# Kernel optimization log

Hardware: AMD Instinct MI355X
Metric: run time of the kernel (lower is better)

## Reference

```python
import jax, jax.numpy as jnp
import numpy as np

SLOPE = 25.0  # snntorch fast_sigmoid default slope
ALPHA = 1.0   # gradient-reversal strength (forward default)

@jax.custom_vjp
def fs_spike(x):
    return (x > 0).astype(x.dtype)
def _fs_fwd(x):
    return (x > 0).astype(x.dtype), x
def _fs_bwd(x, g):
    return (g / (SLOPE * jnp.abs(x) + 1.0) ** 2,)
fs_spike.defvjp(_fs_fwd, _fs_bwd)

@jax.custom_vjp
def atan_spike(x):  # snntorch default ATan surrogate (alpha=2)
    return (x > 0).astype(x.dtype)
def _at_fwd(x):
    return (x > 0).astype(x.dtype), x
def _at_bwd(x, g):
    return (g / (1.0 + (jnp.pi * x) ** 2),)
atan_spike.defvjp(_at_fwd, _at_bwd)

@jax.custom_vjp
def grad_reverse(x):
    return x
def _gr_fwd(x):
    return x, None
def _gr_bwd(_, g):
    return (-ALPHA * g,)
grad_reverse.defvjp(_gr_fwd, _gr_bwd)

def lstm_cell(x, h, c, w_ih, w_hh, b_ih, b_hh):
    gates = x @ w_ih.T + b_ih + h @ w_hh.T + b_hh
    i, f, g, o = jnp.split(gates, 4, axis=-1)
    c_new = jax.nn.sigmoid(f) * c + jax.nn.sigmoid(i) * jnp.tanh(g)
    h_new = jax.nn.sigmoid(o) * jnp.tanh(c_new)
    return h_new, c_new

def slstm_step(x, syn, mem, w_ih, w_hh, b_ih, b_hh, thr):
    # reset computed from previous mem, detached (snntorch mem_reset)
    reset = jax.lax.stop_gradient((mem - thr > 0).astype(mem.dtype))
    h, c = lstm_cell(x, mem, syn, w_ih, w_hh, b_ih, b_hh)
    mem_new = h - reset * thr  # reset_mechanism='subtract'
    spk = fs_spike(mem_new - thr)
    return spk, c, mem_new

def _forward(x, conv_w, bn_gamma, bn_beta, thr_lif1,
             w_ih1, w_hh1, b_ih1, b_hh1, thr1,
             w_ih2, w_hh2, b_ih2, b_hh2, thr2,
             fc_g_w, fc_g_b, fc_d1_w, fc_d1_b, thr_dom, fc_d2_w, fc_d2_b):
    T, B, C = x.shape
    xc = jnp.transpose(x, (1, 2, 0))  # [B, C, T]
    conv = jax.lax.conv_general_dilated(xc, conv_w, window_strides=(1,),
                                        padding=[(2, 2)],
                                        dimension_numbers=('NCH', 'OIH', 'NCH'))
    # BatchNorm1d in training mode: batch stats over (B, T) per channel
    mu = conv.mean(axis=(0, 2), keepdims=True)
    var = conv.var(axis=(0, 2), keepdims=True)
    bn = (conv - mu) / jnp.sqrt(var + 1e-5) * bn_gamma[None, :, None] + bn_beta[None, :, None]
    # Leaky neuron, single step from zero mem: mem = input, spk = fire(mem - thr)
    spk_conv = atan_spike(bn - thr_lif1)
    seq = jnp.transpose(spk_conv, (2, 0, 1))  # [T, B, 64]
    H = w_hh1.shape[1]
    init = (jnp.zeros((B, H), x.dtype), jnp.zeros((B, H), x.dtype),
            jnp.zeros((B, H), x.dtype), jnp.zeros((B, H), x.dtype))

    def step(carry, xt):
        syn1, mem1, syn2, mem2 = carry
        spk1, syn1, mem1 = slstm_step(xt, syn1, mem1, w_ih1, w_hh1, b_ih1, b_hh1, thr1)
        spk2, syn2, mem2 = slstm_step(spk1, syn2, mem2, w_ih2, w_hh2, b_ih2, b_hh2, thr2)
        return (syn1, mem1, syn2, mem2), mem2

    _, mem2_rec = jax.lax.scan(step, init, seq)  # [T, B, H]
    features = mem2_rec.mean(axis=0)             # [B, H]
    gesture = features @ fc_g_w.T + fc_g_b
    rev = grad_reverse(features)
    domain_hidden = atan_spike(rev @ fc_d1_w.T + fc_d1_b - thr_dom)
    domain = domain_hidden @ fc_d2_w.T + fc_d2_b
    return gesture, domain

def setup_inputs() -> dict:
    key = jax.random.key(0)
    ks = jax.random.split(key, 16)
    T, B, C, H = 2000, 256, 14, 128
    f = jnp.float32
    return {
        'x': jax.random.normal(ks[0], (T, B, C), f),
        'conv_w': jax.random.normal(ks[1], (64, C, 5), f) * 0.12,
        'bn_gamma': jnp.ones((64,), f),
        'bn_beta': jnp.zeros((64,), f),
        'thr_lif1': jnp.ones((), f),
        'w_ih1': jax.random.normal(ks[2], (4 * H, 64), f) * 0.08,
        'w_hh1': jax.random.normal(ks[3], (4 * H, H), f) * 0.08,
        'b_ih1': jnp.zeros((4 * H,), f),
        'b_hh1': jnp.zeros((4 * H,), f),
        'thr1': jnp.ones((), f),
        'w_ih2': jax.random.normal(ks[4], (4 * H, H), f) * 0.08,
        'w_hh2': jax.random.normal(ks[5], (4 * H, H), f) * 0.08,
        'b_ih2': jnp.zeros((4 * H,), f),
        'b_hh2': jnp.zeros((4 * H,), f),
        'thr2': jnp.ones((), f),
        'fc_g_w': jax.random.normal(ks[6], (8, H), f) * 0.08,
        'fc_g_b': jnp.zeros((8,), f),
        'fc_d1_w': jax.random.normal(ks[7], (64, H), f) * 0.08,
        'fc_d1_b': jnp.zeros((64,), f),
        'thr_dom': jnp.ones((), f),
        'fc_d2_w': jax.random.normal(ks[8], (10, 64), f) * 0.1,
        'fc_d2_b': jnp.zeros((10,), f),
    }

def reference(x, conv_w, bn_gamma, bn_beta, thr_lif1,
              w_ih1, w_hh1, b_ih1, b_hh1, thr1,
              w_ih2, w_hh2, b_ih2, b_hh2, thr2,
              fc_g_w, fc_g_b, fc_d1_w, fc_d1_b, thr_dom, fc_d2_w, fc_d2_b):
    return _forward(x, conv_w, bn_gamma, bn_beta, thr_lif1,
                    w_ih1, w_hh1, b_ih1, b_hh1, thr1,
                    w_ih2, w_hh2, b_ih2, b_hh2, thr2,
                    fc_g_w, fc_g_b, fc_d1_w, fc_d1_b, thr_dom, fc_d2_w, fc_d2_b)
```

## Files before the change

### kernel.cpp

```cpp
#include <hip/hip_runtime.h>
#include <cstdint>
#include <cstddef>

#define TSTEPS 2000
#define NB     256
#define HID    128
#define CIN    14
#define NGRP   64
#define RG     4
#define BPG    4

#define OFF_CNT   0ull
#define OFF_M1WS  8192ull
#define OFF_M2WS  (OFF_M1WS + 262144ull)
#define OFF_SPKW  (OFF_M2WS + 262144ull)
#define OFF_FEAT  (OFF_SPKW + 8192ull)
#define OFF_AB    (OFF_FEAT + 131072ull)
#define OFF_PART  (OFF_AB   + 512ull)
#define OFF_MASK  (OFF_PART + 1179648ull)
#define ZERO_WORDS 133120

__global__ __launch_bounds__(256) void k0_zero(unsigned* ws) {
  int i = blockIdx.x * 256 + threadIdx.x;
  if (i < ZERO_WORDS) ws[i] = 0u;
}

__global__ __launch_bounds__(256) void k1_stats(const float* __restrict__ x,
                                                const float* __restrict__ cw,
                                                float* __restrict__ part) {
  __shared__ float xLds[244 * CIN];
  __shared__ float cwLds[64 * 70];
  __shared__ float red[2][4][64];
  const int b = blockIdx.x, tile = blockIdx.y;
  const int base = tile * 240;
  for (int f = threadIdx.x; f < 244 * CIN; f += 256) {
    int u = f / CIN, ci = f - u * CIN;
    int tp = base + u - 2;
    xLds[f] = (tp >= 0 && tp < TSTEPS) ? x[((size_t)tp * NB + b) * CIN + ci] : 0.0f;
  }
  for (int f = threadIdx.x; f < 64 * 70; f += 256) cwLds[f] = cw[f];
  __syncthreads();

  const int co = threadIdx.x & 63, tq = threadIdx.x >> 6;
  float cwr[70];
#pragma unroll
  for (int s = 0; s < 70; ++s) cwr[s] = cwLds[co * 70 + s];
  float xw[5][CIN];
  const int u0 = tq * 60;
#pragma unroll
  for (int r = 0; r < 4; ++r)
#pragma unroll
    for (int ci = 0; ci < CIN; ++ci) xw[r][ci] = xLds[(u0 + r) * CIN + ci];

  float s1 = 0.0f, s2 = 0.0f;
  const int tbase = base + tq * 60;
  for (int i5 = 0; i5 < 60; i5 += 5) {
#pragma unroll
    for (int s = 0; s < 5; ++s) {
#pragma unroll
      for (int ci = 0; ci < CIN; ++ci)
        xw[(s + 4) % 5][ci] = xLds[(u0 + i5 + s + 4) * CIN + ci];
      float y = 0.0f;
#pragma unroll
      for (int kk = 0; kk < 5; ++kk)
#pragma unroll
        for (int ci = 0; ci < CIN; ++ci)
          y += xw[(s + kk) % 5][ci] * cwr[ci * 5 + kk];
      if (tbase + i5 + s < TSTEPS) { s1 += y; s2 += y * y; }
    }
  }
  red[0][tq][co] = s1; red[1][tq][co] = s2;
  __syncthreads();
  if (threadIdx.x < 64) {
    float a1 = red[0][0][co] + red[0][1][co] + red[0][2][co] + red[0][3][co];
    float a2 = red[1][0][co] + red[1][1][co] + red[1][2][co] + red[1][3][co];
    int blk = tile * NB + b;
    part[blk * 128 + co * 2 + 0] = a1;
    part[blk * 128 + co * 2 + 1] = a2;
  }
}

__global__ __launch_bounds__(256) void k1b_reduce(const float* __restrict__ gamma,
                           const float* __restrict__ beta,
                           const float* __restrict__ part, float* __restrict__ ab) {
  __shared__ float red[2][4][64];
  const int co = threadIdx.x & 63, pt = threadIdx.x >> 6;
  float s1 = 0.0f, s2 = 0.0f;
  for (int blk = pt * 576; blk < pt * 576 + 576; ++blk) {
    s1 += part[blk * 128 + co * 2 + 0];
    s2 += part[blk * 128 + co * 2 + 1];
  }
  red[0][pt][co] = s1; red[1][pt][co] = s2;
  __syncthreads();
  if (threadIdx.x < 64) {
    float a1 = red[0][0][co] + red[0][1][co] + red[0][2][co] + red[0][3][co];
    float a2 = red[1][0][co] + red[1][1][co] + red[1][2][co] + red[1][3][co];
    const float N = (float)TSTEPS * (float)NB;
    float mu = a1 / N;
    float var = a2 / N - mu * mu;
    float rstd = 1.0f / sqrtf(var + 1e-5f);
    float a = gamma[co] * rstd;
    ab[co] = a;
    ab[64 + co] = beta[co] - mu * a;
  }
}

__global__ __launch_bounds__(256) void k2_spike(const float* __restrict__ x,
                                                const float* __restrict__ cw,
                                                const float* __restrict__ thrp,
                                                const float* __restrict__ ab,
                                                unsigned long long* __restrict__ masks) {
  __shared__ float xLds[244 * CIN];
  __shared__ float cwLds[64 * 70];
  const int b = blockIdx.x, tile = blockIdx.y;
  const int base = tile * 240;
  for (int f = threadIdx.x; f < 244 * CIN; f += 256) {
    int u = f / CIN, ci = f - u * CIN;
    int tp = base + u - 2;
    xLds[f] = (tp >= 0 && tp < TSTEPS) ? x[((size_t)tp * NB + b) * CIN + ci] : 0.0f;
  }
  for (int f = threadIdx.x; f < 64 * 70; f += 256) cwLds[f] = cw[f];
  __syncthreads();

  const int co = threadIdx.x & 63, tq = threadIdx.x >> 6;
  const float thr = thrp[0];
  const float aC = ab[co], bC = ab[64 + co];
  float cwr[70];
#pragma unroll
  for (int s = 0; s < 70; ++s) cwr[s] = cwLds[co * 70 + s];
  float xw[5][CIN];
  const int u0 = tq * 60;
#pragma unroll
  for (int r = 0; r < 4; ++r)
#pragma unroll
    for (int ci = 0; ci < CIN; ++ci) xw[r][ci] = xLds[(u0 + r) * CIN + ci];

  const int tbase = base + tq * 60;
  for (int i5 = 0; i5 < 60; i5 += 5) {
#pragma unroll
    for (int s = 0; s < 5; ++s) {
#pragma unroll
      for (int ci = 0; ci < CIN; ++ci)
        xw[(s + 4) % 5][ci] = xLds[(u0 + i5 + s + 4) * CIN + ci];
      float y = 0.0f;
#pragma unroll
      for (int kk = 0; kk < 5; ++kk)
#pragma unroll
        for (int ci = 0; ci < CIN; ++ci)
          y += xw[(s + kk) % 5][ci] * cwr[ci * 5 + kk];
      int t = tbase + i5 + s;
      if (t < TSTEPS) {
        float bn = y * aC + bC;
        unsigned long long m = __ballot(bn - thr > 0.0f);
        if (co == 0) masks[(size_t)t * NB + b] = m;
      }
    }
  }
}

__global__ __launch_bounds__(512) void kp_fused(char* ws,
    const float* __restrict__ w_ih1, const float* __restrict__ w_hh1,
    const float* __restrict__ b_ih1, const float* __restrict__ b_hh1,
    const float* __restrict__ thr1p,
    const float* __restrict__ w_ih2, const float* __restrict__ w_hh2,
    const float* __restrict__ b_ih2, const float* __restrict__ b_hh2,
    const float* __restrict__ thr2p) {
  __shared__ __align__(16) float A1[192 * 4];
  __shared__ __align__(16) float A2[256 * 4];
  __shared__ float gate1L[128 * 5];
  __shared__ float gate2L[128 * 5];
  __shared__ float biasL1[128], biasL2[128];

  const int tid = threadIdx.x;
  const int bid = blockIdx.x;
  const int g = bid & 63;
  const int q = bid >> 6;
  const int lane = tid & 63, wv = tid >> 6;
  const int idx = lane & 15, kq = lane >> 4;
  const int a = idx & 3, hlq = idx >> 2;
  const int hl = hlq * 8 + wv;
  const int j = a * 32 + hl;
  const int grow = a * 128 + q * 32 + hl;

  unsigned* flags = (unsigned*)(ws + OFF_CNT);
  float* m1ws = (float*)(ws + OFF_M1WS);
  float* m2ws = (float*)(ws + OFF_M2WS);
  unsigned* spkw = (unsigned*)(ws + OFF_SPKW);
  float* feat = (float*)(ws + OFF_FEAT);
  const unsigned long long* masks = (const unsigned long long*)(ws + OFF_MASK);

  float wr1[48];
#pragma unroll
  for (int i = 0; i < 48; ++i) {
    int k = ((i >> 1) << 3) + (kq << 1) + (i & 1);
    wr1[i] = (k < 64) ? w_ih1[grow * 64 + k] : w_hh1[grow * 128 + (k - 64)];
  }
  float wr2[64];
#pragma unroll
  for (int i = 0; i < 64; ++i) {
    int k = ((i >> 1) << 3) + (kq << 1) + (i & 1);
    wr2[i] = (k < 128) ? w_ih2[grow * 128 + k] : w_hh2[grow * 128 + (k - 128)];
  }
  if (tid < 128) {
    int aa = tid >> 5, h2 = tid & 31;
    int gr = aa * 128 + q * 32 + h2;
    biasL1[tid] = b_ih1[gr] + b_hh1[gr];
    biasL2[tid] = b_ih2[gr] + b_hh2[gr];
  }
  const float thr1 = thr1p[0], thr2 = thr2p[0];
  const int cr = tid >> 5, chl = tid & 31;
  float syn1 = 0.0f, mem1 = 0.0f, syn2 = 0.0f, mem2 = 0.0f, facc = 0.0f;
  __syncthreads();

  unsigned long long mrow = masks[(size_t)0 * NB + g * RG + (tid & 3)];

  for (int p = 0; p <= TSTEPS; ++p) {
    const int rb1 = (p + 1) & 1;
    const int wb = p & 1;

    {
      int k = tid >> 2, e = tid & 3;
      float v;
      if (k < 64) v = (float)((mrow >> k) & 1ull);
      else v = __hip_atomic_load(&m1ws[((rb1 * 64 + g) * 4 + e) * 128 + (k - 64)],
                                 __ATOMIC_RELAXED, __HIP_MEMORY_SCOPE_AGENT);
      A1[tid] = v;
    }
    {
      int f = tid + 512;
      if (f < 768) {
        int k = f >> 2, e = f & 3;
        float v = __hip_atomic_load(&m1ws[((rb1 * 64 + g) * 4 + e) * 128 + (k - 64)],
                                    __ATOMIC_RELAXED, __HIP_MEMORY_SCOPE_AGENT);
        A1[f] = v;
      }
    }
    {
      int k = tid >> 2, e = tid & 3;
      unsigned u = __hip_atomic_load(&spkw[((rb1 * 64 + g) * 4 + e) * 4 + (k >> 5)],
                                     __ATOMIC_RELAXED, __HIP_MEMORY_SCOPE_AGENT);
      A2[tid] = (float)((u >> (k & 31)) & 1u);
    }
    {
      int f = tid + 512;
      int k = f >> 2, e = f & 3;
      float v = __hip_atomic_load(&m2ws[((wb * 64 + g) * 4 + e) * 128 + (k - 128)],
                                  __ATOMIC_RELAXED, __HIP_MEMORY_SCOPE_AGENT);
      A2[f] = v;
    }
    if (p + 1 < TSTEPS) mrow = masks[(size_t)(p + 1) * NB + g * RG + (tid & 3)];
    __syncthreads();

    {
      float ac0 = 0.0f, ac1 = 0.0f, ac2 = 0.0f, ac3 = 0.0f;
      const float* Ab = A1 + (kq << 3);
#pragma unroll
      for (int m = 0; m < 24; ++m) {
#pragma unroll
        for (int b2 = 0; b2 < 2; ++b2) {
          float4 av = *(const float4*)(Ab + m * 32 + b2 * 4);
          float w = wr1[m * 2 + b2];
          ac0 += w * av.x; ac1 += w * av.y; ac2 += w * av.z; ac3 += w * av.w;
        }
      }
      ac0 += __shfl_xor(ac0, 16); ac1 += __shfl_xor(ac1, 16);
      ac2 += __shfl_xor(ac2, 16); ac3 += __shfl_xor(ac3, 16);
      ac0 += __shfl_xor(ac0, 32); ac1 += __shfl_xor(ac1, 32);
      ac2 += __shfl_xor(ac2, 32); ac3 += __shfl_xor(ac3, 32);
      if (kq == 0) {
        gate1L[j * 5 + 0] = ac0; gate1L[j * 5 + 1] = ac1;
        gate1L[j * 5 + 2] = ac2; gate1L[j * 5 + 3] = ac3;
      }
    }
    {
      float ac0 = 0.0f, ac1 = 0.0f, ac2 = 0.0f, ac3 = 0.0f;
      const float* Ab = A2 + (kq << 3);
#pragma unroll
      for (int m = 0; m < 32; ++m) {
#pragma unroll
        for (int b2 = 0; b2 < 2; ++b2) {
          float4 av = *(const float4*)(Ab + m * 32 + b2 * 4);
          float w = wr2[m * 2 + b2];
          ac0 += w * av.x; ac1 += w * av.y; ac2 += w * av.z; ac3 += w * av.w;
        }
      }
      ac0 += __shfl_xor(ac0, 16); ac1 += __shfl_xor(ac1, 16);
      ac2 += __shfl_xor(ac2, 16); ac3 += __shfl_xor(ac3, 16);
      ac0 += __shfl_xor(ac0, 32); ac1 += __shfl_xor(ac1, 32);
      ac2 += __shfl_xor(ac2, 32); ac3 += __shfl_xor(ac3, 32);
      if (kq == 0) {
        gate2L[j * 5 + 0] = ac0; gate2L[j * 5 + 1] = ac1;
        gate2L[j * 5 + 2] = ac2; gate2L[j * 5 + 3] = ac3;
      }
    }
    __syncthreads();

    if (tid < 128 && p < TSTEPS) {
      float g0 = biasL1[chl]       + gate1L[(chl) * 5 + cr];
      float g1 = biasL1[32 + chl]  + gate1L[(32 + chl) * 5 + cr];
      float g2 = biasL1[64 + chl]  + gate1L[(64 + chl) * 5 + cr];
      float g3 = biasL1[96 + chl]  + gate1L[(96 + chl) * 5 + cr];
      float rst = (mem1 - thr1 > 0.0f) ? thr1 : 0.0f;
      float ig = 1.0f / (1.0f + expf(-g0));
      float fg = 1.0f / (1.0f + expf(-g1));
      float gg = tanhf(g2);
      float og = 1.0f / (1.0f + expf(-g3));
      float cn = fg * syn1 + ig * gg;
      float mn = og * tanhf(cn) - rst;
      syn1 = cn; mem1 = mn;
      __hip_atomic_store(&m1ws[((wb * 64 + g) * 4 + cr) * 128 + (q * 32 + chl)],
                         mn, __ATOMIC_RELAXED, __HIP_MEMORY_SCOPE_AGENT);
      unsigned long long bal = __ballot(mn - thr1 > 0.0f);
      if (lane == 0)
        __hip_atomic_store(&spkw[((wb * 64 + g) * 4 + (wv * 2 + 0)) * 4 + q],
                           (unsigned)(bal & 0xffffffffull),
                           __ATOMIC_RELAXED, __HIP_MEMORY_SCOPE_AGENT);
      if (lane == 32)
        __hip_atomic_store(&spkw[((wb * 64 + g) * 4 + (wv * 2 + 1)) * 4 + q],
                           (unsigned)(bal >> 32),
                           __ATOMIC_RELAXED, __HIP_MEMORY_SCOPE_AGENT);
    }
    if (tid < 128 && p >= 1) {
      float g0 = biasL2[chl]       + gate2L[(chl) * 5 + cr];
      float g1 = biasL2[32 + chl]  + gate2L[(32 + chl) * 5 + cr];
      float g2 = biasL2[64 + chl]  + gate2L[(64 + chl) * 5 + cr];
      float g3 = biasL2[96 + chl]  + gate2L[(96 + chl) * 5 + cr];
      float rst = (mem2 - thr2 > 0.0f) ? thr2 : 0.0f;
      float ig = 1.0f / (1.0f + expf(-g0));
      float fg = 1.0f / (1.0f + expf(-g1));
      float gg = tanhf(g2);
      float og = 1.0f / (1.0f + expf(-g3));
      float cn = fg * syn2 + ig * gg;
      float mn = og * tanhf(cn) - rst;
      syn2 = cn; mem2 = mn;
      __hip_atomic_store(&m2ws[((rb1 * 64 + g) * 4 + cr) * 128 + (q * 32 + chl)],
                         mn, __ATOMIC_RELAXED, __HIP_MEMORY_SCOPE_AGENT);
      facc += mn;
    }
    __syncthreads();

    if (p < TSTEPS) {
      if (tid == 0)
        __hip_atomic_store(&flags[(g * 4 + q) * 8], (unsigned)(p + 1),
                           __ATOMIC_RELAXED, __HIP_MEMORY_SCOPE_AGENT);
      if (tid < 4) {
        while (__hip_atomic_load(&flags[(g * 4 + tid) * 8],
                                 __ATOMIC_RELAXED, __HIP_MEMORY_SCOPE_AGENT)
               < (unsigned)(p + 1))
          __builtin_amdgcn_s_sleep(1);
      }
      __syncthreads();
    }
  }

  if (tid < 128)
    feat[(g * RG + cr) * 128 + q * 32 + chl] = facc * (1.0f / (float)TSTEPS);
}

__global__ __launch_bounds__(128) void k3_head(const float* __restrict__ feat,
    const float* __restrict__ gw, const float* __restrict__ gb,
    const float* __restrict__ d1w, const float* __restrict__ d1b,
    const float* __restrict__ thrdp,
    const float* __restrict__ d2w, const float* __restrict__ d2b,
    float* __restrict__ out) {
  __shared__ float fL[128];
  __shared__ float dh[64];
  const int b = blockIdx.x, t = threadIdx.x;
  fL[t] = feat[b * 128 + t];
  __syncthreads();
  if (t < 64) {
    float s = d1b[t];
    for (int k = 0; k < 128; ++k) s += d1w[t * 128 + k] * fL[k];
    dh[t] = (s - thrdp[0] > 0.0f) ? 1.0f : 0.0f;
  }
  __syncthreads();
  if (t < 8) {
    float s = gb[t];
    for (int k = 0; k < 128; ++k) s += gw[t * 128 + k] * fL[k];
    out[b * 8 + t] = s;
  }
  if (t >= 64 && t < 74) {
    const int o = t - 64;
    float s = d2b[o];
    for (int k = 0; k < 64; ++k) s += d2w[o * 64 + k] * dh[k];
    out[2048 + b * 10 + o] = s;
  }
}

extern "C" void kernel_launch(void* const* d_in, const int* in_sizes, int n_in,
                              void* d_out, int out_size, void* d_ws, size_t ws_size,
                              hipStream_t stream) {
  const float* x      = (const float*)d_in[0];
  const float* conv_w = (const float*)d_in[1];
  const float* bn_g   = (const float*)d_in[2];
  const float* bn_b   = (const float*)d_in[3];
  const float* thrl1  = (const float*)d_in[4];
  const float* w_ih1  = (const float*)d_in[5];
  const float* w_hh1  = (const float*)d_in[6];
  const float* b_ih1  = (const float*)d_in[7];
  const float* b_hh1  = (const float*)d_in[8];
  const float* thr1   = (const float*)d_in[9];
  const float* w_ih2  = (const float*)d_in[10];
  const float* w_hh2  = (const float*)d_in[11];
  const float* b_ih2  = (const float*)d_in[12];
  const float* b_hh2  = (const float*)d_in[13];
  const float* thr2   = (const float*)d_in[14];
  const float* fc_g_w = (const float*)d_in[15];
  const float* fc_g_b = (const float*)d_in[16];
  const float* fc_d1w = (const float*)d_in[17];
  const float* fc_d1b = (const float*)d_in[18];
  const float* thrdom = (const float*)d_in[19];
  const float* fc_d2w = (const float*)d_in[20];
  const float* fc_d2b = (const float*)d_in[21];
  float* out = (float*)d_out;
  char* ws = (char*)d_ws;

  k0_zero<<<(ZERO_WORDS + 255) / 256, 256, 0, stream>>>((unsigned*)ws);
  k1_stats<<<dim3(NB, 9), 256, 0, stream>>>(x, conv_w, (float*)(ws + OFF_PART));
  k1b_reduce<<<1, 256, 0, stream>>>(bn_g, bn_b, (const float*)(ws + OFF_PART),
                                    (float*)(ws + OFF_AB));
  k2_spike<<<dim3(NB, 9), 256, 0, stream>>>(x, conv_w, thrl1,
                                            (const float*)(ws + OFF_AB),
                                            (unsigned long long*)(ws + OFF_MASK));
  kp_fused<<<NGRP * BPG, 512, 0, stream>>>(ws, w_ih1, w_hh1, b_ih1, b_hh1, thr1,
                                           w_ih2, w_hh2, b_ih2, b_hh2, thr2);
  k3_head<<<NB, 128, 0, stream>>>((const float*)(ws + OFF_FEAT), fc_g_w, fc_g_b,
                                  fc_d1w, fc_d1b, thrdom, fc_d2w, fc_d2b, out);
}
```

Baseline: 17.46 ms.

## Remap persistent LSTM matvec to two rows per thread, coalesce state layout, spin without sleep

Each thread now handles two gate rows, with the K dimension split 8 ways instead of 4. This lets every float4 LDS read of the activation tile feed two weight rows, so LDS traffic per FMA is halved. The layer-1 and layer-2 membrane workspaces are reordered to [hidden][batch] so each thread gathers with one contiguous coalesced atomic load. The inter-block flag spin loop drops s_sleep to cut barrier latency. A 80KB dynamic shared allocation is requested, which likely limits residency to one block per CU, and the extra reduction shuffle step adds some cost.

Measured after the change: 24.35 ms. +39.4%, slower.

```diff
diff --git a/kernel.cpp b/kernel.cpp
--- a/kernel.cpp
+++ b/kernel.cpp
@@ -165,8 +165,9 @@
     const float* __restrict__ w_ih2, const float* __restrict__ w_hh2,
     const float* __restrict__ b_ih2, const float* __restrict__ b_hh2,
     const float* __restrict__ thr2p) {
-  __shared__ __align__(16) float A1[192 * 4];
-  __shared__ __align__(16) float A2[256 * 4];
+  extern __shared__ float dynbuf[];
+  float* A1 = dynbuf;
+  float* A2 = dynbuf + 768;
   __shared__ float gate1L[128 * 5];
   __shared__ float gate2L[128 * 5];
   __shared__ float biasL1[128], biasL2[128];
@@ -176,11 +177,8 @@
   const int g = bid & 63;
   const int q = bid >> 6;
   const int lane = tid & 63, wv = tid >> 6;
-  const int idx = lane & 15, kq = lane >> 4;
-  const int a = idx & 3, hlq = idx >> 2;
-  const int hl = hlq * 8 + wv;
-  const int j = a * 32 + hl;
-  const int grow = a * 128 + q * 32 + hl;
+  const int u = lane & 7, kq = lane >> 3;
+  const int jl0 = wv * 16 + u * 2;
 
   unsigned* flags = (unsigned*)(ws + OFF_CNT);
   float* m1ws = (float*)(ws + OFF_M1WS);
@@ -189,17 +187,22 @@
   float* feat = (float*)(ws + OFF_FEAT);
   const unsigned long long* masks = (const unsigned long long*)(ws + OFF_MASK);
 
-  float wr1[48];
-#pragma unroll
-  for (int i = 0; i < 48; ++i) {
-    int k = ((i >> 1) << 3) + (kq << 1) + (i & 1);
-    wr1[i] = (k < 64) ? w_ih1[grow * 64 + k] : w_hh1[grow * 128 + (k - 64)];
-  }
-  float wr2[64];
-#pragma unroll
-  for (int i = 0; i < 64; ++i) {
-    int k = ((i >> 1) << 3) + (kq << 1) + (i & 1);
-    wr2[i] = (k < 128) ? w_ih2[grow * 128 + k] : w_hh2[grow * 128 + (k - 128)];
+  float wr1[2][24], wr2[2][32];
+#pragma unroll
+  for (int jj = 0; jj < 2; ++jj) {
+    const int j = jl0 + jj;
+    const int a = j >> 5, hl = j & 31;
+    const int grow = a * 128 + q * 32 + hl;
+#pragma unroll
+    for (int m = 0; m < 24; ++m) {
+      int k = m * 8 + kq;
+      wr1[jj][m] = (k < 64) ? w_ih1[grow * 64 + k] : w_hh1[grow * 128 + (k - 64)];
+    }
+#pragma unroll
+    for (int m = 0; m < 32; ++m) {
+      int k = m * 8 + kq;
+      wr2[jj][m] = (k < 128) ? w_ih2[grow * 128 + k] : w_hh2[grow * 128 + (k - 128)];
+    }
   }
   if (tid < 128) {
     int aa = tid >> 5, h2 = tid & 31;
@@ -218,79 +221,90 @@
     const int rb1 = (p + 1) & 1;
     const int wb = p & 1;
 
+    if (tid < 256) {
+      A1[tid] = (float)((mrow >> (tid >> 2)) & 1ull);
+    }
+    {
+      float v = __hip_atomic_load(&m1ws[(size_t)(rb1 * 64 + g) * 512 + tid],
+                                  __ATOMIC_RELAXED, __HIP_MEMORY_SCOPE_AGENT);
+      A1[256 + tid] = v;
+    }
     {
       int k = tid >> 2, e = tid & 3;
-      float v;
-      if (k < 64) v = (float)((mrow >> k) & 1ull);
-      else v = __hip_atomic_load(&m1ws[((rb1 * 64 + g) * 4 + e) * 128 + (k - 64)],
-                                 __ATOMIC_RELAXED, __HIP_MEMORY_SCOPE_AGENT);
-      A1[tid] = v;
+      unsigned uu = __hip_atomic_load(&spkw[((rb1 * 64 + g) * 4 + e) * 4 + (k >> 5)],
+                                      __ATOMIC_RELAXED, __HIP_MEMORY_SCOPE_AGENT);
+      A2[tid] = (float)((uu >> (k & 31)) & 1u);
     }
     {
-      int f = tid + 512;
-      if (f < 768) {
-        int k = f >> 2, e = f & 3;
-        float v = __hip_atomic_load(&m1ws[((rb1 * 64 + g) * 4 + e) * 128 + (k - 64)],
-                                    __ATOMIC_RELAXED, __HIP_MEMORY_SCOPE_AGENT);
-        A1[f] = v;
-      }
-    }
-    {
-      int k = tid >> 2, e = tid & 3;
-      unsigned u = __hip_atomic_load(&spkw[((rb1 * 64 + g) * 4 + e) * 4 + (k >> 5)],
-                                     __ATOMIC_RELAXED, __HIP_MEMORY_SCOPE_AGENT);
-      A2[tid] = (float)((u >> (k & 31)) & 1u);
-    }
-    {
-      int f = tid + 512;
-      int k = f >> 2, e = f & 3;
-      float v = __hip_atomic_load(&m2ws[((wb * 64 + g) * 4 + e) * 128 + (k - 128)],
+      float v = __hip_atomic_load(&m2ws[(size_t)(wb * 64 + g) * 512 + tid],
                                   __ATOMIC_RELAXED, __HIP_MEMORY_SCOPE_AGENT);
-      A2[f] = v;
+      A2[512 + tid] = v;
     }
     if (p + 1 < TSTEPS) mrow = masks[(size_t)(p + 1) * NB + g * RG + (tid & 3)];
     __syncthreads();
 
     {
-      float ac0 = 0.0f, ac1 = 0.0f, ac2 = 0.0f, ac3 = 0.0f;
-      const float* Ab = A1 + (kq << 3);
+      float ac[2][4];
+#pragma unroll
+      for (int jj = 0; jj < 2; ++jj)
+#pragma unroll
+        for (int r = 0; r < 4; ++r) ac[jj][r] = 0.0f;
+      const float4* A1v = (const float4*)A1;
 #pragma unroll
       for (int m = 0; m < 24; ++m) {
-#pragma unroll
-        for (int b2 = 0; b2 < 2; ++b2) {
-          float4 av = *(const float4*)(Ab + m * 32 + b2 * 4);
-          float w = wr1[m * 2 + b2];
-          ac0 += w * av.x; ac1 += w * av.y; ac2 += w * av.z; ac3 += w * av.w;
+        float4 av = A1v[m * 8 + kq];
+        float w0 = wr1[0][m], w1 = wr1[1][m];
+        ac[0][0] += w0 * av.x; ac[0][1] += w0 * av.y;
+        ac[0][2] += w0 * av.z; ac[0][3] += w0 * av.w;
+        ac[1][0] += w1 * av.x; ac[1][1] += w1 * av.y;
+        ac[1][2] += w1 * av.z; ac[1][3] += w1 * av.w;
+      }
+#pragma unroll
+      for (int jj = 0; jj < 2; ++jj)
+#pragma unroll
+        for (int r = 0; r < 4; ++r) {
+          float v = ac[jj][r];
+          v += __shfl_xor(v, 8); v += __shfl_xor(v, 16); v += __shfl_xor(v, 32);
+          ac[jj][r] = v;
         }
-      }
-      ac0 += __shfl_xor(ac0, 16); ac1 += __shfl_xor(ac1, 16);
-      ac2 += __shfl_xor(ac2, 16); ac3 += __shfl_xor(ac3, 16);
-      ac0 += __shfl_xor(ac0, 32); ac1 += __shfl_xor(ac1, 32);
-      ac2 += __shfl_xor(ac2, 32); ac3 += __shfl_xor(ac3, 32);
       if (kq == 0) {
-        gate1L[j * 5 + 0] = ac0; gate1L[j * 5 + 1] = ac1;
-        gate1L[j * 5 + 2] = ac2; gate1L[j * 5 + 3] = ac3;
+#pragma unroll
+        for (int jj = 0; jj < 2; ++jj)
+#pragma unroll
+          for (int r = 0; r < 4; ++r)
+            gate1L[(jl0 + jj) * 5 + r] = ac[jj][r];
       }
     }
     {
-      float ac0 = 0.0f, ac1 = 0.0f, ac2 = 0.0f, ac3 = 0.0f;
-      const float* Ab = A2 + (kq << 3);
+      float ac[2][4];
+#pragma unroll
+      for (int jj = 0; jj < 2; ++jj)
+#pragma unroll
+        for (int r = 0; r < 4; ++r) ac[jj][r] = 0.0f;
+      const float4* A2v = (const float4*)A2;
 #pragma unroll
       for (int m = 0; m < 32; ++m) {
-#pragma unroll
-        for (int b2 = 0; b2 < 2; ++b2) {
-          float4 av = *(const float4*)(Ab + m * 32 + b2 * 4);
-          float w = wr2[m * 2 + b2];
-          ac0 += w * av.x; ac1 += w * av.y; ac2 += w * av.z; ac3 += w * av.w;
+        float4 av = A2v[m * 8 + kq];
+        float w0 = wr2[0][m], w1 = wr2[1][m];
+        ac[0][0] += w0 * av.x; ac[0][1] += w0 * av.y;
+        ac[0][2] += w0 * av.z; ac[0][3] += w0 * av.w;
+        ac[1][0] += w1 * av.x; ac[1][1] += w1 * av.y;
+        ac[1][2] += w1 * av.z; ac[1][3] += w1 * av.w;
+      }
+#pragma unroll
+      for (int jj = 0; jj < 2; ++jj)
+#pragma unroll
+        for (int r = 0; r < 4; ++r) {
+          float v = ac[jj][r];
+          v += __shfl_xor(v, 8); v += __shfl_xor(v, 16); v += __shfl_xor(v, 32);
+          ac[jj][r] = v;
         }
-      }
-      ac0 += __shfl_xor(ac0, 16); ac1 += __shfl_xor(ac1, 16);
-      ac2 += __shfl_xor(ac2, 16); ac3 += __shfl_xor(ac3, 16);
-      ac0 += __shfl_xor(ac0, 32); ac1 += __shfl_xor(ac1, 32);
-      ac2 += __shfl_xor(ac2, 32); ac3 += __shfl_xor(ac3, 32);
       if (kq == 0) {
-        gate2L[j * 5 + 0] = ac0; gate2L[j * 5 + 1] = ac1;
-        gate2L[j * 5 + 2] = ac2; gate2L[j * 5 + 3] = ac3;
+#pragma unroll
+        for (int jj = 0; jj < 2; ++jj)
+#pragma unroll
+          for (int r = 0; r < 4; ++r)
+            gate2L[(jl0 + jj) * 5 + r] = ac[jj][r];
       }
     }
     __syncthreads();
@@ -308,7 +322,7 @@
       float cn = fg * syn1 + ig * gg;
       float mn = og * tanhf(cn) - rst;
       syn1 = cn; mem1 = mn;
-      __hip_atomic_store(&m1ws[((wb * 64 + g) * 4 + cr) * 128 + (q * 32 + chl)],
+      __hip_atomic_store(&m1ws[(size_t)(wb * 64 + g) * 512 + (q * 32 + chl) * 4 + cr],
                          mn, __ATOMIC_RELAXED, __HIP_MEMORY_SCOPE_AGENT);
       unsigned long long bal = __ballot(mn - thr1 > 0.0f);
       if (lane == 0)
@@ -333,7 +347,7 @@
       float cn = fg * syn2 + ig * gg;
       float mn = og * tanhf(cn) - rst;
       syn2 = cn; mem2 = mn;
-      __hip_atomic_store(&m2ws[((rb1 * 64 + g) * 4 + cr) * 128 + (q * 32 + chl)],
+      __hip_atomic_store(&m2ws[(size_t)(rb1 * 64 + g) * 512 + (q * 32 + chl) * 4 + cr],
                          mn, __ATOMIC_RELAXED, __HIP_MEMORY_SCOPE_AGENT);
       facc += mn;
     }
@@ -346,8 +360,7 @@
       if (tid < 4) {
         while (__hip_atomic_load(&flags[(g * 4 + tid) * 8],
                                  __ATOMIC_RELAXED, __HIP_MEMORY_SCOPE_AGENT)
-               < (unsigned)(p + 1))
-          __builtin_amdgcn_s_sleep(1);
+               < (unsigned)(p + 1)) {  }
       }
       __syncthreads();
     }
@@ -422,8 +435,8 @@
   k2_spike<<<dim3(NB, 9), 256, 0, stream>>>(x, conv_w, thrl1,
                                             (const float*)(ws + OFF_AB),
                                             (unsigned long long*)(ws + OFF_MASK));
-  kp_fused<<<NGRP * BPG, 512, 0, stream>>>(ws, w_ih1, w_hh1, b_ih1, b_hh1, thr1,
-                                           w_ih2, w_hh2, b_ih2, b_hh2, thr2);
+  kp_fused<<<NGRP * BPG, 512, 81920, stream>>>(ws, w_ih1, w_hh1, b_ih1, b_hh1, thr1,
+                                               w_ih2, w_hh2, b_ih2, b_hh2, thr2);
   k3_head<<<NB, 128, 0, stream>>>((const float*)(ws + OFF_FEAT), fc_g_w, fc_g_b,
                                   fc_d1w, fc_d1b, thrdom, fc_d2w, fc_d2b, out);
 }
```

## Replace per-step flag barrier with step-tagged 64-bit state words

Applied to the files above, without the earlier changes.

The per-step group barrier (flag store, then a spin on four flags, then an extra __syncthreads) is removed. Instead, every exchanged state value (layer-1 mem, spike bits, layer-2 mem) is packed with its step number into a 64-bit atomic word, and consumers spin until each word carries the expected tag. The state arrays are relaid so each thread loads one contiguous word, and the zeroing kernel now clears only the state region and runs after the mask kernel so it can reuse the space of the stats partials. This aims to cut barrier round-trip latency on every recurrent step, at the cost of twice the exchange traffic and per-thread spin loops.

Result: slower. 21.17 ms (+21.2%).

```diff
diff --git a/kernel.cpp b/kernel.cpp
--- a/kernel.cpp
+++ b/kernel.cpp
@@ -1,6 +1,8 @@
 #include <hip/hip_runtime.h>
 #include <cstdint>
 #include <cstddef>
+
+typedef unsigned long long u64;
 
 #define TSTEPS 2000
 #define NB     256
@@ -8,21 +10,19 @@
 #define CIN    14
 #define NGRP   64
 #define RG     4
-#define BPG    4
-
-#define OFF_CNT   0ull
-#define OFF_M1WS  8192ull
-#define OFF_M2WS  (OFF_M1WS + 262144ull)
-#define OFF_SPKW  (OFF_M2WS + 262144ull)
-#define OFF_FEAT  (OFF_SPKW + 8192ull)
-#define OFF_AB    (OFF_FEAT + 131072ull)
-#define OFF_PART  (OFF_AB   + 512ull)
+
+#define OFF_FEAT  0ull
+#define OFF_AB    131072ull
+#define OFF_M1    131584ull
+#define OFF_M2    (OFF_M1 + 524288ull)
+#define OFF_SPK   (OFF_M2 + 524288ull)
+#define OFF_PART  131584ull
 #define OFF_MASK  (OFF_PART + 1179648ull)
-#define ZERO_WORDS 133120
-
-__global__ __launch_bounds__(256) void k0_zero(unsigned* ws) {
+#define STATE_WORDS 266240
+
+__global__ __launch_bounds__(256) void k0z(unsigned* st) {
   int i = blockIdx.x * 256 + threadIdx.x;
-  if (i < ZERO_WORDS) ws[i] = 0u;
+  if (i < STATE_WORDS) st[i] = 0u;
 }
 
 __global__ __launch_bounds__(256) void k1_stats(const float* __restrict__ x,
@@ -109,7 +109,7 @@
                                                 const float* __restrict__ cw,
                                                 const float* __restrict__ thrp,
                                                 const float* __restrict__ ab,
-                                                unsigned long long* __restrict__ masks) {
+                                                u64* __restrict__ masks) {
   __shared__ float xLds[244 * CIN];
   __shared__ float cwLds[64 * 70];
   const int b = blockIdx.x, tile = blockIdx.y;
@@ -151,11 +151,18 @@
       int t = tbase + i5 + s;
       if (t < TSTEPS) {
         float bn = y * aC + bC;
-        unsigned long long m = __ballot(bn - thr > 0.0f);
+        u64 m = __ballot(bn - thr > 0.0f);
         if (co == 0) masks[(size_t)t * NB + b] = m;
       }
     }
   }
+}
+
+__device__ __forceinline__ u64 ld_agent(const u64* p_) {
+  return __hip_atomic_load(p_, __ATOMIC_RELAXED, __HIP_MEMORY_SCOPE_AGENT);
+}
+__device__ __forceinline__ void st_agent(u64* p_, u64 v) {
+  __hip_atomic_store(p_, v, __ATOMIC_RELAXED, __HIP_MEMORY_SCOPE_AGENT);
 }
 
 __global__ __launch_bounds__(512) void kp_fused(char* ws,
@@ -182,12 +189,11 @@
   const int j = a * 32 + hl;
   const int grow = a * 128 + q * 32 + hl;
 
-  unsigned* flags = (unsigned*)(ws + OFF_CNT);
-  float* m1ws = (float*)(ws + OFF_M1WS);
-  float* m2ws = (float*)(ws + OFF_M2WS);
-  unsigned* spkw = (unsigned*)(ws + OFF_SPKW);
+  u64* m1ws = (u64*)(ws + OFF_M1);
+  u64* m2ws = (u64*)(ws + OFF_M2);
+  u64* spkw = (u64*)(ws + OFF_SPK);
   float* feat = (float*)(ws + OFF_FEAT);
-  const unsigned long long* masks = (const unsigned long long*)(ws + OFF_MASK);
+  const u64* masks = (const u64*)(ws + OFF_MASK);
 
   float wr1[48];
 #pragma unroll
@@ -212,47 +218,36 @@
   float syn1 = 0.0f, mem1 = 0.0f, syn2 = 0.0f, mem2 = 0.0f, facc = 0.0f;
   __syncthreads();
 
-  unsigned long long mrow = masks[(size_t)0 * NB + g * RG + (tid & 3)];
+  u64 mrow = masks[(size_t)0 * NB + g * RG + (tid & 3)];
 
   for (int p = 0; p <= TSTEPS; ++p) {
     const int rb1 = (p + 1) & 1;
     const int wb = p & 1;
-
-    {
-      int k = tid >> 2, e = tid & 3;
-      float v;
-      if (k < 64) v = (float)((mrow >> k) & 1ull);
-      else v = __hip_atomic_load(&m1ws[((rb1 * 64 + g) * 4 + e) * 128 + (k - 64)],
-                                 __ATOMIC_RELAXED, __HIP_MEMORY_SCOPE_AGENT);
-      A1[tid] = v;
-    }
-    {
-      int f = tid + 512;
-      if (f < 768) {
-        int k = f >> 2, e = f & 3;
-        float v = __hip_atomic_load(&m1ws[((rb1 * 64 + g) * 4 + e) * 128 + (k - 64)],
-                                    __ATOMIC_RELAXED, __HIP_MEMORY_SCOPE_AGENT);
-        A1[f] = v;
-      }
-    }
-    {
-      int k = tid >> 2, e = tid & 3;
-      unsigned u = __hip_atomic_load(&spkw[((rb1 * 64 + g) * 4 + e) * 4 + (k >> 5)],
-                                     __ATOMIC_RELAXED, __HIP_MEMORY_SCOPE_AGENT);
-      A2[tid] = (float)((u >> (k & 31)) & 1u);
-    }
-    {
-      int f = tid + 512;
-      int k = f >> 2, e = f & 3;
-      float v = __hip_atomic_load(&m2ws[((wb * 64 + g) * 4 + e) * 128 + (k - 128)],
-                                  __ATOMIC_RELAXED, __HIP_MEMORY_SCOPE_AGENT);
-      A2[f] = v;
-    }
+    const unsigned tagp = (unsigned)p;
+    const u64 wtag = ((u64)(p + 1)) << 32;
+
+    const u64* p1 = m1ws + (size_t)(rb1 * 64 + g) * 512 + tid;
+    const u64* ps = spkw + (size_t)(rb1 * 64 + g) * 16 + (tid & 3) * 4 + (tid >> 7);
+    const u64* p2 = m2ws + (size_t)(wb * 64 + g) * 512 + tid;
+    u64 w1 = ld_agent(p1);
+    u64 wsp = ld_agent(ps);
+    u64 w2 = ld_agent(p2);
+    while ((unsigned)(w1 >> 32) < tagp) { __builtin_amdgcn_s_sleep(1); w1 = ld_agent(p1); }
+    while ((unsigned)(wsp >> 32) < tagp) { __builtin_amdgcn_s_sleep(1); wsp = ld_agent(ps); }
+    while ((unsigned)(w2 >> 32) < tagp) { __builtin_amdgcn_s_sleep(1); w2 = ld_agent(p2); }
+    if (tid < 256) A1[tid] = (float)((mrow >> (tid >> 2)) & 1ull);
+    A1[256 + tid] = __uint_as_float((unsigned)w1);
+    A2[tid] = (float)(((unsigned)wsp >> ((tid >> 2) & 31)) & 1u);
+    A2[512 + tid] = __uint_as_float((unsigned)w2);
     if (p + 1 < TSTEPS) mrow = masks[(size_t)(p + 1) * NB + g * RG + (tid & 3)];
     __syncthreads();
 
     {
-      float ac0 = 0.0f, ac1 = 0.0f, ac2 = 0.0f, ac3 = 0.0f;
+      float ac[4][4];
+#pragma unroll
+      for (int aa = 0; aa < 4; ++aa)
+#pragma unroll
+        for (int r = 0; r < 4; ++r) ac[aa][r] = 0.0f;
       const float* Ab = A1 + (kq << 3);
 #pragma unroll
       for (int m = 0; m < 24; ++m) {
@@ -260,16 +255,19 @@
         for (int b2 = 0; b2 < 2; ++b2) {
           float4 av = *(const float4*)(Ab + m * 32 + b2 * 4);
           float w = wr1[m * 2 + b2];
-          ac0 += w * av.x; ac1 += w * av.y; ac2 += w * av.z; ac3 += w * av.w;
+          ac[0][0] += w * av.x; ac[0][1] += w * av.y;
+          ac[0][2] += w * av.z; ac[0][3] += w * av.w;
         }
       }
-      ac0 += __shfl_xor(ac0, 16); ac1 += __shfl_xor(ac1, 16);
-      ac2 += __shfl_xor(ac2, 16); ac3 += __shfl_xor(ac3, 16);
-      ac0 += __shfl_xor(ac0, 32); ac1 += __shfl_xor(ac1, 32);
-      ac2 += __shfl_xor(ac2, 32); ac3 += __shfl_xor(ac3, 32);
+#pragma unroll
+      for (int r = 0; r < 4; ++r) {
+        float v = ac[0][r];
+        v += __shfl_xor(v, 16); v += __shfl_xor(v, 32);
+        ac[0][r] = v;
+      }
       if (kq == 0) {
-        gate1L[j * 5 + 0] = ac0; gate1L[j * 5 + 1] = ac1;
-        gate1L[j * 5 + 2] = ac2; gate1L[j * 5 + 3] = ac3;
+        gate1L[j * 5 + 0] = ac[0][0]; gate1L[j * 5 + 1] = ac[0][1];
+        gate1L[j * 5 + 2] = ac[0][2]; gate1L[j * 5 + 3] = ac[0][3];
       }
     }
     {
@@ -308,49 +306,39 @@
       float cn = fg * syn1 + ig * gg;
       float mn = og * tanhf(cn) - rst;
       syn1 = cn; mem1 = mn;
-      __hip_atomic_store(&m1ws[((wb * 64 + g) * 4 + cr) * 128 + (q * 32 + chl)],
-                         mn, __ATOMIC_RELAXED, __HIP_MEMORY_SCOPE_AGENT);
-      unsigned long long bal = __ballot(mn - thr1 > 0.0f);
+      st_agent(&m1ws[(size_t)(wb * 64 + g) * 512 + (q * 32 + chl) * 4 + cr],
+               wtag | (u64)__float_as_uint(mn));
+      u64 bal = __ballot(mn - thr1 > 0.0f);
       if (lane == 0)
-        __hip_atomic_store(&spkw[((wb * 64 + g) * 4 + (wv * 2 + 0)) * 4 + q],
-                           (unsigned)(bal & 0xffffffffull),
-                           __ATOMIC_RELAXED, __HIP_MEMORY_SCOPE_AGENT);
+        st_agent(&spkw[(size_t)(wb * 64 + g) * 16 + (wv * 2 + 0) * 4 + q],
+                 wtag | (bal & 0xffffffffull));
       if (lane == 32)
-        __hip_atomic_store(&spkw[((wb * 64 + g) * 4 + (wv * 2 + 1)) * 4 + q],
-                           (unsigned)(bal >> 32),
-                           __ATOMIC_RELAXED, __HIP_MEMORY_SCOPE_AGENT);
-    }
-    if (tid < 128 && p >= 1) {
-      float g0 = biasL2[chl]       + gate2L[(chl) * 5 + cr];
-      float g1 = biasL2[32 + chl]  + gate2L[(32 + chl) * 5 + cr];
-      float g2 = biasL2[64 + chl]  + gate2L[(64 + chl) * 5 + cr];
-      float g3 = biasL2[96 + chl]  + gate2L[(96 + chl) * 5 + cr];
-      float rst = (mem2 - thr2 > 0.0f) ? thr2 : 0.0f;
-      float ig = 1.0f / (1.0f + expf(-g0));
-      float fg = 1.0f / (1.0f + expf(-g1));
-      float gg = tanhf(g2);
-      float og = 1.0f / (1.0f + expf(-g3));
-      float cn = fg * syn2 + ig * gg;
-      float mn = og * tanhf(cn) - rst;
-      syn2 = cn; mem2 = mn;
-      __hip_atomic_store(&m2ws[((rb1 * 64 + g) * 4 + cr) * 128 + (q * 32 + chl)],
-                         mn, __ATOMIC_RELAXED, __HIP_MEMORY_SCOPE_AGENT);
-      facc += mn;
+        st_agent(&spkw[(size_t)(wb * 64 + g) * 16 + (wv * 2 + 1) * 4 + q],
+                 wtag | (bal >> 32));
+    }
+    if (tid < 128) {
+      if (p >= 1 && p <= TSTEPS) {
+        float g0 = biasL2[chl]       + gate2L[(chl) * 5 + cr];
+        float g1 = biasL2[32 + chl]  + gate2L[(32 + chl) * 5 + cr];
+        float g2 = biasL2[64 + chl]  + gate2L[(64 + chl) * 5 + cr];
+        float g3 = biasL2[96 + chl]  + gate2L[(96 + chl) * 5 + cr];
+        float rst = (mem2 - thr2 > 0.0f) ? thr2 : 0.0f;
+        float ig = 1.0f / (1.0f + expf(-g0));
+        float fg = 1.0f / (1.0f + expf(-g1));
+        float gg = tanhf(g2);
+        float og = 1.0f / (1.0f + expf(-g3));
+        float cn = fg * syn2 + ig * gg;
+        float mn = og * tanhf(cn) - rst;
+        syn2 = cn; mem2 = mn;
+        st_agent(&m2ws[(size_t)(rb1 * 64 + g) * 512 + (q * 32 + chl) * 4 + cr],
+                 wtag | (u64)__float_as_uint(mn));
+        facc += mn;
+      } else if (p == 0) {
+        st_agent(&m2ws[(size_t)(rb1 * 64 + g) * 512 + (q * 32 + chl) * 4 + cr],
+                 wtag);
+      }
     }
     __syncthreads();
-
-    if (p < TSTEPS) {
-      if (tid == 0)
-        __hip_atomic_store(&flags[(g * 4 + q) * 8], (unsigned)(p + 1),
-                           __ATOMIC_RELAXED, __HIP_MEMORY_SCOPE_AGENT);
-      if (tid < 4) {
-        while (__hip_atomic_load(&flags[(g * 4 + tid) * 8],
-                                 __ATOMIC_RELAXED, __HIP_MEMORY_SCOPE_AGENT)
-               < (unsigned)(p + 1))
-          __builtin_amdgcn_s_sleep(1);
-      }
-      __syncthreads();
-    }
   }
 
   if (tid < 128)
@@ -415,15 +403,15 @@
   float* out = (float*)d_out;
   char* ws = (char*)d_ws;
 
-  k0_zero<<<(ZERO_WORDS + 255) / 256, 256, 0, stream>>>((unsigned*)ws);
   k1_stats<<<dim3(NB, 9), 256, 0, stream>>>(x, conv_w, (float*)(ws + OFF_PART));
   k1b_reduce<<<1, 256, 0, stream>>>(bn_g, bn_b, (const float*)(ws + OFF_PART),
                                     (float*)(ws + OFF_AB));
   k2_spike<<<dim3(NB, 9), 256, 0, stream>>>(x, conv_w, thrl1,
                                             (const float*)(ws + OFF_AB),
-                                            (unsigned long long*)(ws + OFF_MASK));
-  kp_fused<<<NGRP * BPG, 512, 0, stream>>>(ws, w_ih1, w_hh1, b_ih1, b_hh1, thr1,
-                                           w_ih2, w_hh2, b_ih2, b_hh2, thr2);
+                                            (u64*)(ws + OFF_MASK));
+  k0z<<<(STATE_WORDS + 255) / 256, 256, 0, stream>>>((unsigned*)(ws + OFF_M1));
+  kp_fused<<<NGRP * 4, 512, 0, stream>>>(ws, w_ih1, w_hh1, b_ih1, b_hh1, thr1,
+                                         w_ih2, w_hh2, b_ih2, b_hh2, thr2);
   k3_head<<<NB, 128, 0, stream>>>((const float*)(ws + OFF_FEAT), fc_g_w, fc_g_b,
                                   fc_d1w, fc_d1b, thrdom, fc_d2w, fc_d2b, out);
 }
```
